# Performance work log

Hardware: AMD Instinct MI355X
Metric: run time of the kernel (lower is better)

## Reference

```python
import jax, jax.numpy as jnp
import numpy as np

N = 100000    # nodes
E = 800000    # directed edges
EF = 16       # edge features
NF = 1        # node features (forced by the module's MLP-size constraint)
HID = NF * 8  # NNConv out = 8
H1, C1 = 8, 16  # gat1 heads / per-head channels -> 128
NC = 16       # num_classes (gat2: heads=1, out=NC)


def setup_inputs() -> dict:
    key = jax.random.key(0)
    ks = jax.random.split(key, 20)
    s = 0.1
    return {
        "x": jax.random.normal(ks[0], (N, NF), jnp.float32),
        "edge_index": jax.random.randint(ks[1], (2, E), 0, N, jnp.int64),
        "edge_attr": jax.random.normal(ks[2], (E, EF), jnp.float32),
        # edge MLP: Linear(EF,8) -> ReLU -> Linear(8,8)
        "w1": jax.random.normal(ks[3], (EF, HID), jnp.float32) * s,
        "b1": jnp.zeros((HID,), jnp.float32),
        "w2": jax.random.normal(ks[4], (HID, HID), jnp.float32) * s,
        "b2": jnp.zeros((HID,), jnp.float32),
        # NNConv root weight + bias
        "root": jax.random.normal(ks[5], (NF, HID), jnp.float32) * s,
        "nn_bias": jnp.zeros((HID,), jnp.float32),
        # GAT1: in 8 -> 16 ch x 8 heads
        "g1W": jax.random.normal(ks[6], (HID, H1 * C1), jnp.float32) * s,
        "g1as": jax.random.normal(ks[7], (H1, C1), jnp.float32) * s,
        "g1ad": jax.random.normal(ks[8], (H1, C1), jnp.float32) * s,
        "g1b": jnp.zeros((H1 * C1,), jnp.float32),
        # GAT2: in 128 -> NC, 1 head
        "g2W": jax.random.normal(ks[9], (H1 * C1, NC), jnp.float32) * s,
        "g2as": jax.random.normal(ks[10], (1, NC), jnp.float32) * s,
        "g2ad": jax.random.normal(ks[11], (1, NC), jnp.float32) * s,
        "g2b": jnp.zeros((NC,), jnp.float32),
    }


def _gat(h_in, W, a_src, a_dst, bias, src, dst, n, heads, ch):
    # h: [N, heads, ch]
    h = (h_in @ W).reshape(n, heads, ch)
    e_s = jnp.einsum("nhc,hc->nh", h, a_src)   # per-node src logits
    e_d = jnp.einsum("nhc,hc->nh", h, a_dst)
    e = jax.nn.leaky_relu(e_s[src] + e_d[dst], 0.2)      # [E2, heads]
    m = jax.ops.segment_max(e, dst, num_segments=n)      # segment softmax
    e = jnp.exp(e - m[dst])
    z = jax.ops.segment_sum(e, dst, num_segments=n)
    alpha = e / (z[dst] + 1e-16)                          # [E2, heads]
    out = jax.ops.segment_sum(alpha[:, :, None] * h[src], dst, num_segments=n)
    return out.reshape(n, heads * ch) + bias


def reference(x, edge_index, edge_attr, w1, b1, w2, b2, root, nn_bias,
              g1W, g1as, g1ad, g1b, g2W, g2as, g2ad, g2b):
    n = x.shape[0]
    src, dst = edge_index[0], edge_index[1]

    # ---- NNConv (aggr='mean'): per-edge weight from edge MLP ----
    w_e = jax.nn.relu(edge_attr @ w1 + b1) @ w2 + b2      # [E, NF*HID]
    w_e = w_e.reshape(-1, NF, HID)
    msg = jnp.einsum("ei,eio->eo", x[src], w_e)            # [E, HID]
    sums = jax.ops.segment_sum(msg, dst, num_segments=n)
    cnt = jax.ops.segment_sum(jnp.ones((msg.shape[0],), msg.dtype), dst, num_segments=n)
    aggr = sums / jnp.maximum(cnt, 1.0)[:, None]
    h = jax.nn.relu(aggr + x @ root + nn_bias)             # [N, 8]
    # dropout: eval mode -> identity

    # ---- add self-loops (PyG GATConv default) ----
    loops = jnp.arange(n, dtype=src.dtype)
    src2 = jnp.concatenate([src, loops])
    dst2 = jnp.concatenate([dst, loops])

    h = jax.nn.elu(_gat(h, g1W, g1as, g1ad, g1b, src2, dst2, n, H1, C1))  # [N,128]
    out = _gat(h, g2W, g2as, g2ad, g2b, src2, dst2, n, 1, NC)             # [N,16]
    return jax.nn.log_softmax(out, axis=1)
```

## Files before the change

### kernel.cpp

```cpp
#include <hip/hip_runtime.h>
#include <hip/hip_fp16.h>
#include <math.h>

constexpr int NN  = 100000;
constexpr int NE  = 800000;
constexpr int H1 = 8, C1 = 16;
constexpr int D1 = H1 * C1;
constexpr int NC = 16;
constexpr int SCAN_B = 256;
constexpr int SCAN_NB = (NN + SCAN_B - 1) / SCAN_B;

static inline int cdiv(int a, int b) { return (a + b - 1) / b; }

__device__ inline __half2 h2_bits(unsigned u) {
    __half2 r; __builtin_memcpy(&r, &u, 4); return r;
}
__device__ inline __half2 shflx_h2(__half2 v, int off) {
    int iv; __builtin_memcpy(&iv, &v, 4);
    iv = __shfl_xor(iv, off);
    __half2 r; __builtin_memcpy(&r, &iv, 4); return r;
}

__global__ void hist_kernel(const int* __restrict__ dst, int* __restrict__ deg) {
    int e = blockIdx.x * blockDim.x + threadIdx.x;
    if (e < NE) atomicAdd(&deg[dst[e]], 1);
}

__global__ void scan1(const int* __restrict__ deg, int* __restrict__ row,
                      int* __restrict__ partial) {
    __shared__ int s[SCAN_B];
    int tid = threadIdx.x;
    int i = blockIdx.x * SCAN_B + tid;
    int v = (i < NN) ? deg[i] : 0;
    s[tid] = v;
    __syncthreads();
    for (int off = 1; off < SCAN_B; off <<= 1) {
        int t = 0;
        if (tid >= off) t = s[tid - off];
        __syncthreads();
        s[tid] += t;
        __syncthreads();
    }
    if (i < NN) row[i] = s[tid] - v;
    if (tid == SCAN_B - 1) partial[blockIdx.x] = s[tid];
}

__global__ void scan2(int* __restrict__ partial, int nb) {
    __shared__ int s[512];
    int tid = threadIdx.x;
    int v = (tid < nb) ? partial[tid] : 0;
    s[tid] = v;
    __syncthreads();
    for (int off = 1; off < 512; off <<= 1) {
        int t = 0;
        if (tid >= off) t = s[tid - off];
        __syncthreads();
        s[tid] += t;
        __syncthreads();
    }
    if (tid < nb) partial[tid] = s[tid] - v;
}

__global__ void scan3(int* __restrict__ row, const int* __restrict__ partial,
                      int* __restrict__ cursor) {
    int i = blockIdx.x * SCAN_B + threadIdx.x;
    if (i < NN) {
        int r = row[i] + partial[blockIdx.x];
        row[i] = r;
        cursor[i] = r;
    }
}

__global__ void nnconv_scatter(const float* __restrict__ x,
                               const int* __restrict__ src, const int* __restrict__ dst,
                               const float* __restrict__ ea,
                               const float* __restrict__ w1, const float* __restrict__ b1,
                               const float* __restrict__ w2, const float* __restrict__ b2,
                               int* __restrict__ cursor,
                               int* __restrict__ src_s, __half* __restrict__ msg_s) {
    __shared__ float sw1[16 * 8], sw2[8 * 8], sb1[8], sb2[8];
    int t = threadIdx.x;
    if (t < 128) sw1[t] = w1[t];
    else if (t < 192) sw2[t - 128] = w2[t - 128];
    else if (t < 200) sb1[t - 192] = b1[t - 192];
    else if (t < 208) sb2[t - 200] = b2[t - 200];
    __syncthreads();
    int e = blockIdx.x * blockDim.x + t;
    if (e >= NE) return;

    float a[16];
    const float4* ea4 = (const float4*)(ea + (size_t)e * 16);
    float4 v0 = ea4[0], v1 = ea4[1], v2 = ea4[2], v3 = ea4[3];
    a[0]=v0.x; a[1]=v0.y; a[2]=v0.z; a[3]=v0.w;
    a[4]=v1.x; a[5]=v1.y; a[6]=v1.z; a[7]=v1.w;
    a[8]=v2.x; a[9]=v2.y; a[10]=v2.z; a[11]=v2.w;
    a[12]=v3.x; a[13]=v3.y; a[14]=v3.z; a[15]=v3.w;

    float hdn[8];
#pragma unroll
    for (int j = 0; j < 8; j++) {
        float s = sb1[j];
#pragma unroll
        for (int i = 0; i < 16; i++) s = fmaf(a[i], sw1[i * 8 + j], s);
        hdn[j] = fmaxf(s, 0.f);
    }
    int sn = src[e], dn = dst[e];
    float xv = x[sn];
    __align__(16) __half msg[8];
#pragma unroll
    for (int j = 0; j < 8; j++) {
        float s = sb2[j];
#pragma unroll
        for (int i = 0; i < 8; i++) s = fmaf(hdn[i], sw2[i * 8 + j], s);
        msg[j] = __float2half(xv * s);
    }
    int pos = atomicAdd(&cursor[dn], 1);
    src_s[pos] = sn;
    *(uint4*)(msg_s + (size_t)pos * 8) = *(const uint4*)msg;
}

__global__ void fused_node1(const float* __restrict__ x,
                            const int* __restrict__ row, const int* __restrict__ deg,
                            const __half* __restrict__ msg_s,
                            const float* __restrict__ root, const float* __restrict__ nb,
                            const float* __restrict__ W,
                            const float* __restrict__ as_, const float* __restrict__ ad_,
                            __half* __restrict__ h1h,
                            float* __restrict__ es, float* __restrict__ ed) {
    int t = blockIdx.x * blockDim.x + threadIdx.x;
    if (t >= NN * 8) return;
    int n = t >> 3, j = t & 7;
    int rs = row[n], d = deg[n];
    float sum = 0.f;
    for (int p = rs; p < rs + d; p++) sum += __half2float(msg_s[(size_t)p * 8 + j]);
    float hj = fmaxf(sum / fmaxf((float)d, 1.f) + x[n] * root[j] + nb[j], 0.f);

    float hv[8];
#pragma unroll
    for (int k = 0; k < 8; k++) hv[k] = __shfl(hj, k, 8);

    int hd = j;
    float acc[16];
#pragma unroll
    for (int c = 0; c < 16; c++) acc[c] = 0.f;
#pragma unroll
    for (int k = 0; k < 8; k++) {
        const float* wr = W + k * D1 + hd * 16;
#pragma unroll
        for (int c = 0; c < 16; c++) acc[c] = fmaf(hv[k], wr[c], acc[c]);
    }
    float s = 0.f, dd = 0.f;
    __align__(16) __half hh[16];
#pragma unroll
    for (int c = 0; c < 16; c++) {
        s = fmaf(acc[c], as_[hd * 16 + c], s);
        dd = fmaf(acc[c], ad_[hd * 16 + c], dd);
        hh[c] = __float2half(acc[c]);
    }
    float4* hp = (float4*)(h1h + (size_t)n * D1 + hd * 16);
    hp[0] = ((const float4*)hh)[0];
    hp[1] = ((const float4*)hh)[1];
    es[t] = s;
    ed[t] = dd;
}

__global__ __launch_bounds__(256) void gat1_gather(
        const int* __restrict__ row, const int* __restrict__ deg,
        const int* __restrict__ src_s,
        const float* __restrict__ es, const float* __restrict__ ed,
        const __half* __restrict__ h1h, const float* __restrict__ b,
        const float* __restrict__ W2,
        const float* __restrict__ as2, const float* __restrict__ ad2,
        __half* __restrict__ h2h, float* __restrict__ es2, float* __restrict__ ed2) {
    __shared__ float sW2[2048];
    __shared__ float so[4][4][132];
    int tid = threadIdx.x;
    for (int idx = tid; idx < 2048; idx += 256) sW2[idx] = W2[idx];
    __syncthreads();

    int wv = tid >> 6, lane = tid & 63;
    int g  = lane >> 4;
    int cl = lane & 15;
    int hd = cl >> 1;
    const uint4* h1h4 = (const uint4*)h1h;
    float4 bv0 = *((const float4*)(b + cl * 8));
    float4 bv1 = *((const float4*)(b + cl * 8 + 4));

    int base = (blockIdx.x * 4 + wv) * 4;
    for (int i = 0; i < 4; i++) {
        int node = base + i;
        int rs = row[node], d = deg[node];
        float edn = ed[node * 8 + hd];

        float vs = es[node * 8 + hd] + edn;
        vs = fmaxf(vs, 0.2f * vs);
        float a0 = (g == 0) ? __expf(vs) : 0.f;
        float z = a0;
        __half2 ap = __float2half2_rn(a0);
        uint4 gl = h1h4[(unsigned)node * 16u + (unsigned)cl];
        __half2 acc0 = __hmul2(ap, h2_bits(gl.x));
        __half2 acc1 = __hmul2(ap, h2_bits(gl.y));
        __half2 acc2 = __hmul2(ap, h2_bits(gl.z));
        __half2 acc3 = __hmul2(ap, h2_bits(gl.w));

        for (int k = g; k < d; k += 4) {
            int s = src_s[rs + k];
            float v = es[(unsigned)s * 8u + hd] + edn;
            v = fmaxf(v, 0.2f * v);
            float a = __expf(v);
            uint4 ge = h1h4[(unsigned)s * 16u + (unsigned)cl];
            __half2 a2 = __float2half2_rn(a);
            z += a;
            acc0 = __hfma2(a2, h2_bits(ge.x), acc0);
            acc1 = __hfma2(a2, h2_bits(ge.y), acc1);
            acc2 = __hfma2(a2, h2_bits(ge.z), acc2);
            acc3 = __hfma2(a2, h2_bits(ge.w), acc3);
        }
        z += __shfl_xor(z, 16); z += __shfl_xor(z, 32);
        acc0 = __hadd2(acc0, shflx_h2(acc0, 16)); acc0 = __hadd2(acc0, shflx_h2(acc0, 32));
        acc1 = __hadd2(acc1, shflx_h2(acc1, 16)); acc1 = __hadd2(acc1, shflx_h2(acc1, 32));
        acc2 = __hadd2(acc2, shflx_h2(acc2, 16)); acc2 = __hadd2(acc2, shflx_h2(acc2, 32));
        acc3 = __hadd2(acc3, shflx_h2(acc3, 16)); acc3 = __hadd2(acc3, shflx_h2(acc3, 32));

        float rz = 1.f / (z + 1e-16f);
        float2 f0 = __half22float2(acc0), f1 = __half22float2(acc1);
        float2 f2 = __half22float2(acc2), f3 = __half22float2(acc3);
        float o0 = fmaf(f0.x, rz, bv0.x), o1 = fmaf(f0.y, rz, bv0.y);
        float o2 = fmaf(f1.x, rz, bv0.z), o3 = fmaf(f1.y, rz, bv0.w);
        float o4 = fmaf(f2.x, rz, bv1.x), o5 = fmaf(f2.y, rz, bv1.y);
        float o6 = fmaf(f3.x, rz, bv1.z), o7 = fmaf(f3.y, rz, bv1.w);
        o0 = o0 > 0.f ? o0 : expm1f(o0);
        o1 = o1 > 0.f ? o1 : expm1f(o1);
        o2 = o2 > 0.f ? o2 : expm1f(o2);
        o3 = o3 > 0.f ? o3 : expm1f(o3);
        o4 = o4 > 0.f ? o4 : expm1f(o4);
        o5 = o5 > 0.f ? o5 : expm1f(o5);
        o6 = o6 > 0.f ? o6 : expm1f(o6);
        o7 = o7 > 0.f ? o7 : expm1f(o7);
        if (g == 0) {
            float4* sp = (float4*)&so[wv][i][cl * 8];
            sp[0] = make_float4(o0, o1, o2, o3);
            sp[1] = make_float4(o4, o5, o6, o7);
        }
    }
    __asm__ __volatile__("s_waitcnt lgkmcnt(0)" ::: "memory");

    int nl = lane >> 4, c = lane & 15;
    float partial = 0.f;
#pragma unroll 4
    for (int k = 0; k < 128; k += 2) {
        float2 sv = *(const float2*)&so[wv][nl][k];
        partial = fmaf(sv.x, sW2[k * 16 + c], partial);
        partial = fmaf(sv.y, sW2[(k + 1) * 16 + c], partial);
    }
    float ta = partial * as2[c], tb = partial * ad2[c];
#pragma unroll
    for (int off = 1; off < 16; off <<= 1) {
        ta += __shfl_xor(ta, off);
        tb += __shfl_xor(tb, off);
    }
    h2h[(size_t)(base + nl) * 16 + c] = __float2half(partial);
    if (c == 0) { es2[base + nl] = ta; ed2[base + nl] = tb; }
}

__global__ __launch_bounds__(256) void gat2_gather(
        const int* __restrict__ row, const int* __restrict__ deg,
        const int* __restrict__ src_s,
        const float* __restrict__ es, const float* __restrict__ ed,
        const __half* __restrict__ h2h, const float* __restrict__ b,
        float* __restrict__ out) {
    int tid = threadIdx.x;
    int wv = tid >> 6, lane = tid & 63;
    int g = lane >> 3, l = lane & 7;
    const __half2* h2h2 = (const __half2*)h2h;
    float2 bv = ((const float2*)b)[l];
    int base = (blockIdx.x * 4 + wv) * 4;
    for (int i = 0; i < 4; i++) {
        int node = base + i;
        int rs = row[node], d = deg[node];
        float edn = ed[node];
        float vs = es[node] + edn;
        vs = fmaxf(vs, 0.2f * vs);
        float a0 = (g == 0) ? __expf(vs) : 0.f;
        float z = a0;
        __half2 acc = __hmul2(__float2half2_rn(a0), h2h2[(unsigned)node * 8u + l]);

        for (int k = g; k < d; k += 8) {
            int s = src_s[rs + k];
            float v = es[s] + edn;
            v = fmaxf(v, 0.2f * v);
            float a = __expf(v);
            __half2 hv = h2h2[(unsigned)s * 8u + l];
            z += a;
            acc = __hfma2(__float2half2_rn(a), hv, acc);
        }
        z += __shfl_xor(z, 8); z += __shfl_xor(z, 16); z += __shfl_xor(z, 32);
        acc = __hadd2(acc, shflx_h2(acc, 8));
        acc = __hadd2(acc, shflx_h2(acc, 16));
        acc = __hadd2(acc, shflx_h2(acc, 32));

        float rz = 1.f / (z + 1e-16f);
        float2 f = __half22float2(acc);
        float o0 = fmaf(f.x, rz, bv.x);
        float o1 = fmaf(f.y, rz, bv.y);
        float mx = fmaxf(o0, o1);
        mx = fmaxf(mx, __shfl_xor(mx, 1));
        mx = fmaxf(mx, __shfl_xor(mx, 2));
        mx = fmaxf(mx, __shfl_xor(mx, 4));
        float ss = __expf(o0 - mx) + __expf(o1 - mx);
        ss += __shfl_xor(ss, 1); ss += __shfl_xor(ss, 2); ss += __shfl_xor(ss, 4);
        float lg = mx + __logf(ss);
        if (g == 0)
            ((float2*)out)[(unsigned)node * 8u + l] = make_float2(o0 - lg, o1 - lg);
    }
}

extern "C" void kernel_launch(void* const* d_in, const int* in_sizes, int n_in,
                              void* d_out, int out_size, void* d_ws, size_t ws_size,
                              hipStream_t stream) {
    const float* x    = (const float*)d_in[0];
    const int*   ei   = (const int*)d_in[1];
    const float* ea   = (const float*)d_in[2];
    const float* w1   = (const float*)d_in[3];
    const float* b1   = (const float*)d_in[4];
    const float* w2   = (const float*)d_in[5];
    const float* b2   = (const float*)d_in[6];
    const float* root = (const float*)d_in[7];
    const float* nb   = (const float*)d_in[8];
    const float* g1W  = (const float*)d_in[9];
    const float* g1as = (const float*)d_in[10];
    const float* g1ad = (const float*)d_in[11];
    const float* g1b  = (const float*)d_in[12];
    const float* g2W  = (const float*)d_in[13];
    const float* g2as = (const float*)d_in[14];
    const float* g2ad = (const float*)d_in[15];
    const float* g2b  = (const float*)d_in[16];
    float* out = (float*)d_out;

    const int* src = ei;
    const int* dst = ei + NE;

    float* ws = (float*)d_ws;
    size_t o = 0;
    __half* msg_s  = (__half*)(ws + o); o += (size_t)NE * 4;
    __half* h1h    = (__half*)(ws + o); o += (size_t)NN * D1 / 2;
    __half* h2h    = (__half*)(ws + o); o += (size_t)NN * NC / 2;
    int*  src_s = (int*)(ws + o); o += NE;
    int*  deg   = (int*)(ws + o); o += NN;
    int*  row   = (int*)(ws + o); o += NN;
    int*  cur   = (int*)(ws + o); o += NN;
    int*  part  = (int*)(ws + o); o += 512;
    float* es1  = ws + o; o += (size_t)NN * H1;
    float* ed1  = ws + o; o += (size_t)NN * H1;
    float* es2  = ws + o; o += NN;
    float* ed2  = ws + o; o += NN;
    (void)ws_size; (void)in_sizes; (void)n_in; (void)out_size;

    const int B = 256;

    hipMemsetAsync(deg, 0, (size_t)NN * sizeof(int), stream);
    hist_kernel<<<cdiv(NE, B), B, 0, stream>>>(dst, deg);
    scan1<<<SCAN_NB, SCAN_B, 0, stream>>>(deg, row, part);
    scan2<<<1, 512, 0, stream>>>(part, SCAN_NB);
    scan3<<<SCAN_NB, SCAN_B, 0, stream>>>(row, part, cur);

    nnconv_scatter<<<cdiv(NE, B), B, 0, stream>>>(x, src, dst, ea, w1, b1, w2, b2,
                                                  cur, src_s, msg_s);
    fused_node1<<<cdiv(NN * 8, B), B, 0, stream>>>(x, row, deg, msg_s, root, nb,
                                                   g1W, g1as, g1ad, h1h, es1, ed1);
    gat1_gather<<<NN / 16, B, 0, stream>>>(row, deg, src_s, es1, ed1, h1h,
                                           g1b, g2W, g2as, g2ad, h2h, es2, ed2);
    gat2_gather<<<NN / 16, B, 0, stream>>>(row, deg, src_s, es2, ed2, h2h, g2b, out);
}
```

Baseline: 352.8 us.

## Store NNConv messages in edge order and gather via sorted edge ids

Measured after the change: 351.1 us. Within noise of the previous version (-0.5%).

```diff
diff --git a/kernel.cpp b/kernel.cpp
--- a/kernel.cpp
+++ b/kernel.cpp
@@ -11,6 +11,8 @@
 constexpr int SCAN_NB = (NN + SCAN_B - 1) / SCAN_B;
 
 static inline int cdiv(int a, int b) { return (a + b - 1) / b; }
+
+typedef int   v4i __attribute__((ext_vector_type(4)));
 
 __device__ inline __half2 h2_bits(unsigned u) {
     __half2 r; __builtin_memcpy(&r, &u, 4); return r;
@@ -77,7 +79,8 @@
                                const float* __restrict__ w1, const float* __restrict__ b1,
                                const float* __restrict__ w2, const float* __restrict__ b2,
                                int* __restrict__ cursor,
-                               int* __restrict__ src_s, __half* __restrict__ msg_s) {
+                               int* __restrict__ src_s, int* __restrict__ eid_s,
+                               __half* __restrict__ msg_s) {
     __shared__ float sw1[16 * 8], sw2[8 * 8], sb1[8], sb2[8];
     int t = threadIdx.x;
     if (t < 128) sw1[t] = w1[t];
@@ -114,13 +117,16 @@
         for (int i = 0; i < 8; i++) s = fmaf(hdn[i], sw2[i * 8 + j], s);
         msg[j] = __float2half(xv * s);
     }
+    v4i mv; __builtin_memcpy(&mv, msg, 16);
+    __builtin_nontemporal_store(mv, (v4i*)(msg_s + (size_t)e * 8));
     int pos = atomicAdd(&cursor[dn], 1);
     src_s[pos] = sn;
-    *(uint4*)(msg_s + (size_t)pos * 8) = *(const uint4*)msg;
+    eid_s[pos] = e;
 }
 
 __global__ void fused_node1(const float* __restrict__ x,
                             const int* __restrict__ row, const int* __restrict__ deg,
+                            const int* __restrict__ eid_s,
                             const __half* __restrict__ msg_s,
                             const float* __restrict__ root, const float* __restrict__ nb,
                             const float* __restrict__ W,
@@ -131,8 +137,31 @@
     if (t >= NN * 8) return;
     int n = t >> 3, j = t & 7;
     int rs = row[n], d = deg[n];
-    float sum = 0.f;
-    for (int p = rs; p < rs + d; p++) sum += __half2float(msg_s[(size_t)p * 8 + j]);
+
+    float p0 = 0.f, p1 = 0.f, p2 = 0.f, p3 = 0.f;
+    float p4 = 0.f, p5 = 0.f, p6 = 0.f, p7 = 0.f;
+    for (int k = j; k < d; k += 8) {
+        int eid = eid_s[rs + k];
+        uint4 m = *(const uint4*)(msg_s + (size_t)eid * 8);
+        float2 f0 = __half22float2(h2_bits(m.x));
+        float2 f1 = __half22float2(h2_bits(m.y));
+        float2 f2 = __half22float2(h2_bits(m.z));
+        float2 f3 = __half22float2(h2_bits(m.w));
+        p0 += f0.x; p1 += f0.y; p2 += f1.x; p3 += f1.y;
+        p4 += f2.x; p5 += f2.y; p6 += f3.x; p7 += f3.y;
+    }
+    float k0 = (j & 4) ? p4 : p0, s0 = (j & 4) ? p0 : p4;
+    float k1 = (j & 4) ? p5 : p1, s1 = (j & 4) ? p1 : p5;
+    float k2 = (j & 4) ? p6 : p2, s2 = (j & 4) ? p2 : p6;
+    float k3 = (j & 4) ? p7 : p3, s3 = (j & 4) ? p3 : p7;
+    k0 += __shfl_xor(s0, 4); k1 += __shfl_xor(s1, 4);
+    k2 += __shfl_xor(s2, 4); k3 += __shfl_xor(s3, 4);
+    float m0 = (j & 2) ? k2 : k0, n0 = (j & 2) ? k0 : k2;
+    float m1 = (j & 2) ? k3 : k1, n1 = (j & 2) ? k1 : k3;
+    m0 += __shfl_xor(n0, 2); m1 += __shfl_xor(n1, 2);
+    float q  = (j & 1) ? m1 : m0, r = (j & 1) ? m0 : m1;
+    float sum = q + __shfl_xor(r, 1);
+
     float hj = fmaxf(sum / fmaxf((float)d, 1.f) + x[n] * root[j] + nb[j], 0.f);
 
     float hv[8];
@@ -229,14 +258,14 @@
         float o2 = fmaf(f1.x, rz, bv0.z), o3 = fmaf(f1.y, rz, bv0.w);
         float o4 = fmaf(f2.x, rz, bv1.x), o5 = fmaf(f2.y, rz, bv1.y);
         float o6 = fmaf(f3.x, rz, bv1.z), o7 = fmaf(f3.y, rz, bv1.w);
-        o0 = o0 > 0.f ? o0 : expm1f(o0);
-        o1 = o1 > 0.f ? o1 : expm1f(o1);
-        o2 = o2 > 0.f ? o2 : expm1f(o2);
-        o3 = o3 > 0.f ? o3 : expm1f(o3);
-        o4 = o4 > 0.f ? o4 : expm1f(o4);
-        o5 = o5 > 0.f ? o5 : expm1f(o5);
-        o6 = o6 > 0.f ? o6 : expm1f(o6);
-        o7 = o7 > 0.f ? o7 : expm1f(o7);
+        o0 = o0 > 0.f ? o0 : __expf(o0) - 1.f;
+        o1 = o1 > 0.f ? o1 : __expf(o1) - 1.f;
+        o2 = o2 > 0.f ? o2 : __expf(o2) - 1.f;
+        o3 = o3 > 0.f ? o3 : __expf(o3) - 1.f;
+        o4 = o4 > 0.f ? o4 : __expf(o4) - 1.f;
+        o5 = o5 > 0.f ? o5 : __expf(o5) - 1.f;
+        o6 = o6 > 0.f ? o6 : __expf(o6) - 1.f;
+        o7 = o7 > 0.f ? o7 : __expf(o7) - 1.f;
         if (g == 0) {
             float4* sp = (float4*)&so[wv][i][cl * 8];
             sp[0] = make_float4(o0, o1, o2, o3);
@@ -272,7 +301,7 @@
     int tid = threadIdx.x;
     int wv = tid >> 6, lane = tid & 63;
     int g = lane >> 3, l = lane & 7;
-    const __half2* h2h2 = (const __half2*)h2h;
+    const unsigned* h2i = (const unsigned*)h2h;
     float2 bv = ((const float2*)b)[l];
     int base = (blockIdx.x * 4 + wv) * 4;
     for (int i = 0; i < 4; i++) {
@@ -283,16 +312,17 @@
         vs = fmaxf(vs, 0.2f * vs);
         float a0 = (g == 0) ? __expf(vs) : 0.f;
         float z = a0;
-        __half2 acc = __hmul2(__float2half2_rn(a0), h2h2[(unsigned)node * 8u + l]);
+        __half2 acc = __hmul2(__float2half2_rn(a0),
+                              h2_bits(h2i[(unsigned)node * 8u + l]));
 
         for (int k = g; k < d; k += 8) {
             int s = src_s[rs + k];
             float v = es[s] + edn;
             v = fmaxf(v, 0.2f * v);
             float a = __expf(v);
-            __half2 hv = h2h2[(unsigned)s * 8u + l];
+            unsigned hraw = h2i[(unsigned)s * 8u + l];
             z += a;
-            acc = __hfma2(__float2half2_rn(a), hv, acc);
+            acc = __hfma2(__float2half2_rn(a), h2_bits(hraw), acc);
         }
         z += __shfl_xor(z, 8); z += __shfl_xor(z, 16); z += __shfl_xor(z, 32);
         acc = __hadd2(acc, shflx_h2(acc, 8));
@@ -346,6 +376,7 @@
     __half* h1h    = (__half*)(ws + o); o += (size_t)NN * D1 / 2;
     __half* h2h    = (__half*)(ws + o); o += (size_t)NN * NC / 2;
     int*  src_s = (int*)(ws + o); o += NE;
+    int*  eid_s = (int*)(ws + o); o += NE;
     int*  deg   = (int*)(ws + o); o += NN;
     int*  row   = (int*)(ws + o); o += NN;
     int*  cur   = (int*)(ws + o); o += NN;
@@ -365,8 +396,8 @@
     scan3<<<SCAN_NB, SCAN_B, 0, stream>>>(row, part, cur);
 
     nnconv_scatter<<<cdiv(NE, B), B, 0, stream>>>(x, src, dst, ea, w1, b1, w2, b2,
-                                                  cur, src_s, msg_s);
-    fused_node1<<<cdiv(NN * 8, B), B, 0, stream>>>(x, row, deg, msg_s, root, nb,
+                                                  cur, src_s, eid_s, msg_s);
+    fused_node1<<<cdiv(NN * 8, B), B, 0, stream>>>(x, row, deg, eid_s, msg_s, root, nb,
                                                    g1W, g1as, g1ad, h1h, es1, ed1);
     gat1_gather<<<NN / 16, B, 0, stream>>>(row, deg, src_s, es1, ed1, h1h,
                                            g1b, g2W, g2as, g2ad, h2h, es2, ed2);
```
